# Optimization experiments

Measured on AMD Instinct MI355X. Metric: run time of the kernel, lower is better.

Reference implementation:

```python
import jax, jax.numpy as jnp
import numpy as np

COMMITMENT_COST = 0.25
DECAY = 0.99
EPSILON = 1e-05


def setup_inputs() -> dict:
    key = jax.random.key(0)
    k1, k2, k3 = jax.random.split(key, 3)
    B, C, H, W = 64, 64, 64, 64  # C == embedding_dim
    K, D = 1024, 64
    return {
        "inputs": jax.random.normal(k1, (B, C, H, W), dtype=jnp.float32),
        "weight": jax.random.normal(k2, (K, D), dtype=jnp.float32),
        "ema_cluster_size": jnp.ones((K,), dtype=jnp.float32),
        "ema_w": jax.random.normal(k3, (K, D), dtype=jnp.float32),
    }


def reference(inputs, weight, ema_cluster_size, ema_w):
    K, D = weight.shape
    # NCHW -> NHWC, flatten to [N, D]
    x = jnp.transpose(inputs, (0, 2, 3, 1))
    flat = x.reshape(-1, D)
    # squared L2 distances to all codebook entries: [N, K]
    distances = (
        jnp.sum(flat * flat, axis=1, keepdims=True)
        + jnp.sum(weight * weight, axis=1)
        - 2.0 * flat @ weight.T
    )
    idx = jnp.argmin(distances, axis=1)  # [N]
    # training-mode EMA update (replaces the one-hot scatter + matmuls with segment sums)
    counts = jax.ops.segment_sum(jnp.ones_like(idx, dtype=flat.dtype), idx, num_segments=K)
    dw = jax.ops.segment_sum(flat, idx, num_segments=K)  # encodings.T @ flat_input
    cs = ema_cluster_size * DECAY + (1.0 - DECAY) * counts
    n = jnp.sum(cs)
    cs = (cs + EPSILON) / (n + K * EPSILON) * n  # Laplace smoothing
    ew = ema_w * DECAY + (1.0 - DECAY) * dw
    new_weight = ew / cs[:, None]
    # quantize with the UPDATED codebook (matches in-place torch order)
    quantized = new_weight[idx].reshape(x.shape)
    e_latent_loss = jnp.mean(jnp.square(jax.lax.stop_gradient(quantized) - x))
    loss = COMMITMENT_COST * e_latent_loss
    quantized_st = x + jax.lax.stop_gradient(quantized - x)  # straight-through
    return loss, jnp.transpose(quantized_st, (0, 3, 1, 2)), idx[:, None]
```

## Files before the change

kernel.cpp:

```cpp
#include <hip/hip_runtime.h>

#define K_CODES 1024
#define D_DIM   64
#define N_ROWS  262144
#define HW      4096
#define CHW     262144
#define N_ELEM  16777216
#define DECAY   0.99f
#define OMD     0.01f
#define EPS_F   1e-05f
#define MARGIN_BF 0.008f
#define FLAG_CAP 32768
#define SEG_CAP  2048
#define NHB      64
#define BROWS    128

typedef __attribute__((ext_vector_type(8))) short bf16x8;
typedef __attribute__((ext_vector_type(4))) float f32x4;

constexpr size_t OFF_LOSS    = 0;
constexpr size_t OFF_FLAGCNT = 8;
constexpr size_t OFF_DONE    = 12;
constexpr size_t ZERO_BYTES  = 64;
constexpr size_t OFF_W2F     = 64;
constexpr size_t OFF_W2D     = 4160;
constexpr size_t OFF_CS     = 12352;
constexpr size_t OFF_GOFF    = 16448;
constexpr size_t OFF_DW      = 20608;
constexpr size_t OFF_NEWW    = 282752;
constexpr size_t OFF_IDX     = 544896;
constexpr size_t OFF_HISTB   = 1593472;
constexpr size_t OFF_SORT    = 1855616;
constexpr size_t OFF_FLAGS   = 1855616;
constexpr size_t OFF_WFRAG   = 1986688;

__device__ __forceinline__ short f2bf(float f) {
    unsigned u = __float_as_uint(f);
    u += 0x7fffu + ((u >> 16) & 1u);
    return (short)(u >> 16);
}
__device__ __forceinline__ float bf2f(short h) {
    return __uint_as_float(((unsigned)(unsigned short)h) << 16);
}

__device__ __forceinline__ void gload_lds16(const float4* g, void* l) {
    __builtin_amdgcn_global_load_lds(
        (const __attribute__((address_space(1))) void*)g,
        (__attribute__((address_space(3))) void*)l, 16, 0, 0);
}

__global__ __launch_bounds__(256) void prep_kernel(
    const float* __restrict__ w, short* __restrict__ wfrag,
    float* __restrict__ w2f, double* __restrict__ w2d) {
    int t = threadIdx.x;
    if (blockIdx.x < 32) {
        int gid = blockIdx.x * 256 + t;
        int j = gid >> 7, h = (gid >> 6) & 1, L = gid & 63;
        int code = j * 16 + (L & 15);
        int kb = h * 32 + ((L >> 4) << 3);
        const float* wp = w + code * D_DIM + kb;
        short hi[8], lo[8];
#pragma unroll
        for (int i = 0; i < 8; ++i) {
            float v = wp[i];
            short hb = f2bf(v);
            hi[i] = hb;
            lo[i] = f2bf(v - bf2f(hb));
        }
        short* dh = wfrag + (size_t)(((j * 2 + h) * 2 + 0) * 64 + L) * 8;
        short* dl = wfrag + (size_t)(((j * 2 + h) * 2 + 1) * 64 + L) * 8;
#pragma unroll
        for (int i = 0; i < 8; ++i) { dh[i] = hi[i]; dl[i] = lo[i]; }
    } else {
        int k = (blockIdx.x - 32) * 256 + t;
        const float* wk = w + k * D_DIM;
        float sf = 0.f; double sd = 0.0;
#pragma unroll
        for (int d = 0; d < D_DIM; ++d) {
            float wv = wk[d];
            sf = fmaf(wv, wv, sf);
            sd = fma((double)wv, (double)wv, sd);
        }
        w2f[k] = sf; w2d[k] = sd;
    }
}

__global__ __launch_bounds__(256) __attribute__((amdgpu_waves_per_eu(2, 4)))
void argmin_kernel(
    const float* __restrict__ inp, const short* __restrict__ wfrag,
    const float* __restrict__ w2f, int* __restrict__ idx_ws,
    float* __restrict__ out_idx_f, float* __restrict__ xt,
    int* __restrict__ flagcnt, int* __restrict__ flaglist) {
    __shared__ float w2s[K_CODES];
    __shared__ alignas(16) char smem_u[64 * 68 * 4];
    __shared__ alignas(16) short bufA[8192];
    float (*xs)[68] = (float (*)[68])smem_u;
    short* bufB = (short*)smem_u;

    int t = threadIdx.x;
    ((float4*)w2s)[t] = ((const float4*)w2f)[t];

    int rowbase = blockIdx.x * BROWS;
    int b = rowbase >> 12, hwb = rowbase & (HW - 1);
    const float* xp = inp + (size_t)b * CHW + hwb;
    int lane = t & 63, wave = t >> 6;
    int q = lane >> 4, col = lane & 15;

    bf16x8 aH[2][2], aL[2][2];

    for (int p = 0; p < 2; ++p) {
#pragma unroll
        for (int it = 0; it < 16; ++it) {
            int d = wave * 16 + it;
            xs[lane][d] = xp[(size_t)d * HW + p * 64 + lane];
        }
        __syncthreads();

        float4* xt4 = (float4*)(xt + (size_t)(rowbase + p * 64) * D_DIM);
#pragma unroll
        for (int i2 = 0; i2 < 4; ++i2) {
            int c2 = t + i2 * 256;
            xt4[c2] = ((const float4*)xs[c2 >> 4])[c2 & 15];
        }

        if ((wave >> 1) == p) {
#pragma unroll
            for (int s2 = 0; s2 < 2; ++s2) {
                int rl = (wave & 1) * 32 + s2 * 16 + col;
#pragma unroll
                for (int h = 0; h < 2; ++h) {
#pragma unroll
                    for (int i = 0; i < 8; ++i) {
                        float v = xs[rl][h * 32 + q * 8 + i];
                        short hb = f2bf(v);
                        aH[s2][h][i] = hb;
                        aL[s2][h][i] = f2bf(v - bf2f(hb));
                    }
                }
            }
        }
        __syncthreads();
    }

    float best[2][4], best2[2][4];
#pragma unroll
    for (int s2 = 0; s2 < 2; ++s2)
#pragma unroll
        for (int r = 0; r < 4; ++r) { best[s2][r] = 3.4e38f; best2[s2][r] = 3.4e38f; }
    const float4* wsrc = (const float4*)wfrag;

    {
        const float4* src = wsrc + t;
        char* nb = (char*)bufA + wave * 1024;
#pragma unroll
        for (int i2 = 0; i2 < 4; ++i2)
            gload_lds16(src + i2 * 256, nb + i2 * 4096);
    }

    for (int st = 0; st < 16; ++st) {
        asm volatile("s_waitcnt vmcnt(0)" ::: "memory");
        __syncthreads();
        if (st < 15) {
            const float4* src = wsrc + (size_t)(st + 1) * 1024 + t;
            char* nb = ((st & 1) ? (char*)bufA : (char*)bufB) + wave * 1024;
#pragma unroll
            for (int i2 = 0; i2 < 4; ++i2)
                gload_lds16(src + i2 * 256, nb + i2 * 4096);
        }
        const bf16x8* wt = (const bf16x8*)((st & 1) ? bufB : bufA);

#pragma unroll
        for (int jj = 0; jj < 4; ++jj) {
            int j = st * 4 + jj;
            bf16x8 bh0 = wt[(jj * 4 + 0) * 64 + lane];
            bf16x8 bl0 = wt[(jj * 4 + 1) * 64 + lane];
            bf16x8 bh1 = wt[(jj * 4 + 2) * 64 + lane];
            bf16x8 bl1 = wt[(jj * 4 + 3) * 64 + lane];
            f32x4 acc0 = {0.f, 0.f, 0.f, 0.f};
            f32x4 acc1 = {0.f, 0.f, 0.f, 0.f};
            acc0 = __builtin_amdgcn_mfma_f32_16x16x32_bf16(aL[0][0], bh0, acc0, 0, 0, 0);
            acc1 = __builtin_amdgcn_mfma_f32_16x16x32_bf16(aL[1][0], bh0, acc1, 0, 0, 0);
            acc0 = __builtin_amdgcn_mfma_f32_16x16x32_bf16(aL[0][1], bh1, acc0, 0, 0, 0);
            acc1 = __builtin_amdgcn_mfma_f32_16x16x32_bf16(aL[1][1], bh1, acc1, 0, 0, 0);
            acc0 = __builtin_amdgcn_mfma_f32_16x16x32_bf16(aH[0][0], bl0, acc0, 0, 0, 0);
            acc1 = __builtin_amdgcn_mfma_f32_16x16x32_bf16(aH[1][0], bl0, acc1, 0, 0, 0);
            acc0 = __builtin_amdgcn_mfma_f32_16x16x32_bf16(aH[0][1], bl1, acc0, 0, 0, 0);
            acc1 = __builtin_amdgcn_mfma_f32_16x16x32_bf16(aH[1][1], bl1, acc1, 0, 0, 0);
            acc0 = __builtin_amdgcn_mfma_f32_16x16x32_bf16(aH[0][0], bh0, acc0, 0, 0, 0);
            acc1 = __builtin_amdgcn_mfma_f32_16x16x32_bf16(aH[1][0], bh0, acc1, 0, 0, 0);
            acc0 = __builtin_amdgcn_mfma_f32_16x16x32_bf16(aH[0][1], bh1, acc0, 0, 0, 0);
            acc1 = __builtin_amdgcn_mfma_f32_16x16x32_bf16(aH[1][1], bh1, acc1, 0, 0, 0);
            float w2c = w2s[j * 16 + col];
#pragma unroll
            for (int s2 = 0; s2 < 2; ++s2) {
#pragma unroll
                for (int r = 0; r < 4; ++r) {
                    float s = fmaf(-2.f, (s2 ? acc1 : acc0)[r], w2c);
                    float key = __int_as_float(
                        (__float_as_int(s) & ~63) | j);
                    best2[s2][r] = fminf(best2[s2][r], fmaxf(key, best[s2][r]));
                    best[s2][r]  = fminf(best[s2][r], key);
                }
            }
        }
    }

    int bk[2][4];
#pragma unroll
    for (int s2 = 0; s2 < 2; ++s2)
#pragma unroll
        for (int r = 0; r < 4; ++r)
            bk[s2][r] = ((__float_as_int(best[s2][r]) & 63) << 4) | col;

#pragma unroll
    for (int m = 1; m < 16; m <<= 1) {
#pragma unroll
        for (int s2 = 0; s2 < 2; ++s2) {
#pragma unroll
            for (int r = 0; r < 4; ++r) {
                float ob  = __shfl_xor(best[s2][r], m, 64);
                float ob2 = __shfl_xor(best2[s2][r], m, 64);
                int   obk = __shfl_xor(bk[s2][r], m, 64);
                float nb2 = fminf(fminf(best2[s2][r], ob2),
                                  fmaxf(best[s2][r], ob));
                int   nbk = ob < best[s2][r] ? obk
                            : (best[s2][r] < ob ? bk[s2][r]
                                                : min(bk[s2][r], obk));
                best[s2][r]  = fminf(best[s2][r], ob);
                best2[s2][r] = nb2;
                bk[s2][r]    = nbk;
            }
        }
    }

    if (col == 0) {
#pragma unroll
        for (int s2 = 0; s2 < 2; ++s2) {
#pragma unroll
            for (int r = 0; r < 4; ++r) {
                int row = rowbase + wave * 32 + s2 * 16 + q * 4 + r;
                idx_ws[row]    = bk[s2][r];
                out_idx_f[row] = (float)bk[s2][r];
                if (best2[s2][r] - best[s2][r] < MARGIN_BF) {
                    int pos = atomicAdd(flagcnt, 1);
                    if (pos < FLAG_CAP) flaglist[pos] = row;
                }
            }
        }
    }
}

__global__ __launch_bounds__(256) void refine_kernel(
    const float* __restrict__ xt, const float* __restrict__ weight,
    const double* __restrict__ w2d, int* __restrict__ idx_ws,
    float* __restrict__ out_idx_f, const int* __restrict__ flagcnt,
    const int* __restrict__ flaglist) {
    __shared__ float sx[4][64];
    int cnt = *flagcnt;
    if (cnt > FLAG_CAP) cnt = FLAG_CAP;
    int t = threadIdx.x, lane = t & 63, wave = t >> 6;

    for (int r = blockIdx.x * 4 + wave; r < cnt; r += gridDim.x * 4) {
        int row = flaglist[r];
        sx[wave][lane] = xt[(size_t)row * D_DIM + lane];
        asm volatile("s_waitcnt lgkmcnt(0)" ::: "memory");

        double bd = 1.0e300; int bi = 0;
        int k0 = lane * 16;
#pragma unroll 4
        for (int c = 0; c < 16; ++c) {
            int k = k0 + c;
            const float4* wk4 = (const float4*)(weight + (size_t)k * D_DIM);
            double dot = 0.0;
#pragma unroll
            for (int d4 = 0; d4 < 16; ++d4) {
                float4 wv = wk4[d4];
                dot = fma((double)wv.x, (double)sx[wave][d4 * 4 + 0], dot);
                dot = fma((double)wv.y, (double)sx[wave][d4 * 4 + 1], dot);
                dot = fma((double)wv.z, (double)sx[wave][d4 * 4 + 2], dot);
                dot = fma((double)wv.w, (double)sx[wave][d4 * 4 + 3], dot);
            }
            double dist = w2d[k] - 2.0 * dot;
            if (dist < bd) { bd = dist; bi = k; }
        }
#pragma unroll
        for (int m = 1; m < 64; m <<= 1) {
            double od = __shfl_xor(bd, m, 64);
            int    oi = __shfl_xor(bi, m, 64);
            if (od < bd || (od == bd && oi < bi)) { bd = od; bi = oi; }
        }
        if (lane == 0 && bi != idx_ws[row]) {
            idx_ws[row]    = bi;
            out_idx_f[row] = (float)bi;
        }
    }
}

__global__ __launch_bounds__(256) void hist_kernel(
    const int* __restrict__ idx_ws, int* __restrict__ histb) {
    __shared__ int h[K_CODES];
    int t = threadIdx.x, b = blockIdx.x;
    for (int i = t; i < K_CODES; i += 256) h[i] = 0;
    __syncthreads();
    const int4* idx4 = (const int4*)idx_ws + b * 1024;
#pragma unroll
    for (int i = 0; i < 4; ++i) {
        int4 c = idx4[t + i * 256];
        atomicAdd(&h[c.x], 1); atomicAdd(&h[c.y], 1);
        atomicAdd(&h[c.z], 1); atomicAdd(&h[c.w], 1);
    }
    __syncthreads();
    for (int i = t; i < K_CODES; i += 256) histb[b * K_CODES + i] = h[i];
}

__global__ __launch_bounds__(1024) void scan_kernel(
    int* __restrict__ histb, int* __restrict__ goff,
    const float* __restrict__ ema_cs, float* __restrict__ csbuf) {
    __shared__ int pre[K_CODES];
    __shared__ float red[K_CODES];
    int k = threadIdx.x;

    int s = 0;
    for (int b = 0; b < NHB; ++b) {
        int v = histb[b * K_CODES + k];
        histb[b * K_CODES + k] = s;
        s += v;
    }
    int cnt = s;

    pre[k] = cnt;
    __syncthreads();
    for (int d = 1; d < K_CODES; d <<= 1) {
        int v = (k >= d) ? pre[k - d] : 0;
        __syncthreads();
        if (k >= d) pre[k] += v;
        __syncthreads();
    }
    int base = pre[k] - cnt;
    goff[k] = base;
    if (k == K_CODES - 1) goff[K_CODES] = pre[k];

    for (int b = 0; b < NHB; ++b) histb[b * K_CODES + k] += base;

    float cs = ema_cs[k] * DECAY + OMD * (float)cnt;
    red[k] = cs;
    __syncthreads();
    for (int s2 = 512; s2 > 0; s2 >>= 1) {
        if (k < s2) red[k] += red[k + s2];
        __syncthreads();
    }
    float n = red[0];
    csbuf[k] = (cs + EPS_F) / (n + (float)K_CODES * EPS_F) * n;
}

__global__ __launch_bounds__(256) void scatter_kernel(
    const int* __restrict__ idx_ws, const int* __restrict__ histb,
    int* __restrict__ sorted) {
    __shared__ int cur[K_CODES];
    int t = threadIdx.x, b = blockIdx.x;
    for (int i = t; i < K_CODES; i += 256) cur[i] = histb[b * K_CODES + i];
    __syncthreads();
    const int4* idx4 = (const int4*)idx_ws + b * 1024;
#pragma unroll
    for (int i = 0; i < 4; ++i) {
        int4 c = idx4[t + i * 256];
        int r0 = (b * 1024 + t + i * 256) * 4;
        sorted[atomicAdd(&cur[c.x], 1)] = r0 + 0;
        sorted[atomicAdd(&cur[c.y], 1)] = r0 + 1;
        sorted[atomicAdd(&cur[c.z], 1)] = r0 + 2;
        sorted[atomicAdd(&cur[c.w], 1)] = r0 + 3;
    }
}

__global__ __launch_bounds__(256) void dwred_kernel(
    const float* __restrict__ xt, const int* __restrict__ sorted,
    const int* __restrict__ goff, const float* __restrict__ ema_w,
    const float* __restrict__ csbuf, float* __restrict__ new_w) {
    __shared__ int   rows[SEG_CAP];
    __shared__ float red[256];
    int k = blockIdx.x, t = threadIdx.x;
    int base = goff[k];
    int cnt = goff[k + 1] - base;
    int cc = cnt > SEG_CAP ? SEG_CAP : cnt;

    for (int i = t; i < cc; i += 256) rows[i] = sorted[base + i];
    __syncthreads();

    int d = t & 63, sub = t >> 6;
    float a0 = 0.f, a1 = 0.f;
    int i = sub;
    for (; i + 4 < cc; i += 8) {
        a0 += xt[(size_t)rows[i] * D_DIM + d];
        a1 += xt[(size_t)rows[i + 4] * D_DIM + d];
    }
    for (; i < cc; i += 4) a0 += xt[(size_t)rows[i] * D_DIM + d];
    red[t] = a0 + a1;
    __syncthreads();
    if (t < 64) {
        float dwv = red[t] + red[t + 64] + red[t + 128] + red[t + 192];
        new_w[k * D_DIM + t] =
            (ema_w[k * D_DIM + t] * DECAY + OMD * dwv) / csbuf[k];
    }
}

__global__ __launch_bounds__(256) void out_kernel(
    const float* __restrict__ inp, const float* __restrict__ new_w,
    const int* __restrict__ idx_ws, float* __restrict__ out,
    double* __restrict__ loss_acc, int* __restrict__ done_cnt) {
    int row = blockIdx.x * 256 + threadIdx.x;
    int b  = row >> 12;
    int hw = row & (HW - 1);
    const float* xp = inp + (size_t)b * CHW + hw;
    float* op = out + 1 + (size_t)b * CHW + hw;

    int k = idx_ws[row];
    const float* q = new_w + k * D_DIM;

    float lsum = 0.f;
#pragma unroll
    for (int d = 0; d < D_DIM; ++d) {
        float xv = xp[(size_t)d * HW];
        float qv = q[d];
        float diff = qv - xv;
        lsum = fmaf(diff, diff, lsum);
        op[(size_t)d * HW] = xv + diff;
    }

    __shared__ double lred[256];
    lred[threadIdx.x] = (double)lsum;
    __syncthreads();
    for (int s = 128; s > 0; s >>= 1) {
        if (threadIdx.x < s) lred[threadIdx.x] += lred[threadIdx.x + s];
        __syncthreads();
    }
    if (threadIdx.x == 0) {
        atomicAdd(loss_acc, lred[0]);
        __threadfence();
        int old = atomicAdd(done_cnt, 1);
        if (old == (int)gridDim.x - 1) {
            double v = atomicAdd(loss_acc, 0.0);
            out[0] = (float)(0.25 * (v / (double)N_ELEM));
        }
    }
}

extern "C" void kernel_launch(void* const* d_in, const int* in_sizes, int n_in,
                              void* d_out, int out_size, void* d_ws, size_t ws_size,
                              hipStream_t stream) {
    const float* inp    = (const float*)d_in[0];
    const float* weight = (const float*)d_in[1];
    const float* ema_cs = (const float*)d_in[2];
    const float* ema_w  = (const float*)d_in[3];
    float* out = (float*)d_out;

    char* ws = (char*)d_ws;
    double* loss_acc = (double*)(ws + OFF_LOSS);
    int*    flagcnt  = (int*)(ws + OFF_FLAGCNT);
    int*    done_cnt = (int*)(ws + OFF_DONE);
    float*  w2f      = (float*)(ws + OFF_W2F);
    double* w2d      = (double*)(ws + OFF_W2D);
    float*  csbuf    = (float*)(ws + OFF_CS);
    int*    goff     = (int*)(ws + OFF_GOFF);
    float*  new_w    = (float*)(ws + OFF_NEWW);
    int*    idx_ws   = (int*)(ws + OFF_IDX);
    int*    histb    = (int*)(ws + OFF_HISTB);
    int*    sorted   = (int*)(ws + OFF_SORT);
    int*    flaglist = (int*)(ws + OFF_FLAGS);
    short*  wfrag    = (short*)(ws + OFF_WFRAG);

    float* xt        = out + 1;
    float* out_idx_f = out + 1 + (size_t)N_ELEM;

    hipMemsetAsync(ws, 0, ZERO_BYTES, stream);

    prep_kernel<<<36, 256, 0, stream>>>(weight, wfrag, w2f, w2d);

    argmin_kernel<<<N_ROWS / BROWS, 256, 0, stream>>>(
        inp, wfrag, w2f, idx_ws, out_idx_f, xt, flagcnt, flaglist);

    refine_kernel<<<256, 256, 0, stream>>>(
        xt, weight, w2d, idx_ws, out_idx_f, flagcnt, flaglist);

    hist_kernel<<<NHB, 256, 0, stream>>>(idx_ws, histb);

    scan_kernel<<<1, 1024, 0, stream>>>(histb, goff, ema_cs, csbuf);

    scatter_kernel<<<NHB, 256, 0, stream>>>(idx_ws, histb, sorted);

    dwred_kernel<<<K_CODES, 256, 0, stream>>>(xt, sorted, goff, ema_w, csbuf, new_w);

    out_kernel<<<N_ROWS / 256, 256, 0, stream>>>(inp, new_w, idx_ws, out,
                                                 loss_acc, done_cnt);
}
```

Measured before the change: 436.1 us.

## Enlarge argmin row tile, fold norm into MFMA init, fuse scan into hist

The argmin kernel now handles 256 rows per block, so each wave keeps 64 rows (4 A-fragment sets) and every codebook fragment loaded from LDS is reused across more rows. The accumulator starts at -0.5*||w||^2, so the argmin becomes a max of x·w - 0.5||w||^2 and the per-element fma disappears, and the ambiguity margin is halved to match the halved scale. The scan kernel is merged into the last-finishing hist block through an atomic done counter. The memset is replaced by zeroing inside prep_kernel, and refine gets twice as many blocks. The cost is higher register pressure and fewer argmin blocks, plus a serial tail in the last hist block.

```diff
diff --git a/kernel.cpp b/kernel.cpp
--- a/kernel.cpp
+++ b/kernel.cpp
@@ -9,11 +9,11 @@
 #define DECAY   0.99f
 #define OMD     0.01f
 #define EPS_F   1e-05f
-#define MARGIN_BF 0.008f
+#define MARGIN_ACC 0.004f
 #define FLAG_CAP 32768
 #define SEG_CAP  2048
 #define NHB      64
-#define BROWS    128
+#define BROWS    256
 
 typedef __attribute__((ext_vector_type(8))) short bf16x8;
 typedef __attribute__((ext_vector_type(4))) float f32x4;
@@ -21,12 +21,11 @@
 constexpr size_t OFF_LOSS    = 0;
 constexpr size_t OFF_FLAGCNT = 8;
 constexpr size_t OFF_DONE    = 12;
-constexpr size_t ZERO_BYTES  = 64;
+constexpr size_t OFF_HDONE   = 16;
 constexpr size_t OFF_W2F     = 64;
 constexpr size_t OFF_W2D     = 4160;
 constexpr size_t OFF_CS     = 12352;
 constexpr size_t OFF_GOFF    = 16448;
-constexpr size_t OFF_DW      = 20608;
 constexpr size_t OFF_NEWW    = 282752;
 constexpr size_t OFF_IDX     = 544896;
 constexpr size_t OFF_HISTB   = 1593472;
@@ -51,8 +50,10 @@
 
 __global__ __launch_bounds__(256) void prep_kernel(
     const float* __restrict__ w, short* __restrict__ wfrag,
-    float* __restrict__ w2f, double* __restrict__ w2d) {
+    float* __restrict__ w2f, double* __restrict__ w2d,
+    int* __restrict__ zero16) {
     int t = threadIdx.x;
+    if (blockIdx.x == 35 && t < 8) zero16[t] = 0;
     if (blockIdx.x < 32) {
         int gid = blockIdx.x * 256 + t;
         int j = gid >> 7, h = (gid >> 6) & 1, L = gid & 63;
@@ -85,7 +86,7 @@
     }
 }
 
-__global__ __launch_bounds__(256) __attribute__((amdgpu_waves_per_eu(2, 4)))
+__global__ __launch_bounds__(256) __attribute__((amdgpu_waves_per_eu(3, 4)))
 void argmin_kernel(
     const float* __restrict__ inp, const short* __restrict__ wfrag,
     const float* __restrict__ w2f, int* __restrict__ idx_ws,
@@ -106,9 +107,10 @@
     int lane = t & 63, wave = t >> 6;
     int q = lane >> 4, col = lane & 15;
 
-    bf16x8 aH[2][2], aL[2][2];
-
-    for (int p = 0; p < 2; ++p) {
+    bf16x8 aH[4][2], aL[4][2];
+
+#pragma unroll
+    for (int p = 0; p < 4; ++p) {
 #pragma unroll
         for (int it = 0; it < 16; ++it) {
             int d = wave * 16 + it;
@@ -123,10 +125,10 @@
             xt4[c2] = ((const float4*)xs[c2 >> 4])[c2 & 15];
         }
 
-        if ((wave >> 1) == p) {
-#pragma unroll
-            for (int s2 = 0; s2 < 2; ++s2) {
-                int rl = (wave & 1) * 32 + s2 * 16 + col;
+        if (wave == p) {
+#pragma unroll
+            for (int s2 = 0; s2 < 4; ++s2) {
+                int rl = s2 * 16 + col;
 #pragma unroll
                 for (int h = 0; h < 2; ++h) {
 #pragma unroll
@@ -142,11 +144,11 @@
         __syncthreads();
     }
 
-    float best[2][4], best2[2][4];
-#pragma unroll
-    for (int s2 = 0; s2 < 2; ++s2)
-#pragma unroll
-        for (int r = 0; r < 4; ++r) { best[s2][r] = 3.4e38f; best2[s2][r] = 3.4e38f; }
+    float best[4][4], best2[4][4];
+#pragma unroll
+    for (int s2 = 0; s2 < 4; ++s2)
+#pragma unroll
+        for (int r = 0; r < 4; ++r) { best[s2][r] = -3.4e38f; best2[s2][r] = -3.4e38f; }
     const float4* wsrc = (const float4*)wfrag;
 
     {
@@ -156,6 +158,8 @@
         for (int i2 = 0; i2 < 4; ++i2)
             gload_lds16(src + i2 * 256, nb + i2 * 4096);
     }
+
+#define MFMA16(A, B, C) __builtin_amdgcn_mfma_f32_16x16x32_bf16(A, B, C, 0, 0, 0)
 
     for (int st = 0; st < 16; ++st) {
         asm volatile("s_waitcnt vmcnt(0)" ::: "memory");
@@ -176,38 +180,38 @@
             bf16x8 bl0 = wt[(jj * 4 + 1) * 64 + lane];
             bf16x8 bh1 = wt[(jj * 4 + 2) * 64 + lane];
             bf16x8 bl1 = wt[(jj * 4 + 3) * 64 + lane];
-            f32x4 acc0 = {0.f, 0.f, 0.f, 0.f};
-            f32x4 acc1 = {0.f, 0.f, 0.f, 0.f};
-            acc0 = __builtin_amdgcn_mfma_f32_16x16x32_bf16(aL[0][0], bh0, acc0, 0, 0, 0);
-            acc1 = __builtin_amdgcn_mfma_f32_16x16x32_bf16(aL[1][0], bh0, acc1, 0, 0, 0);
-            acc0 = __builtin_amdgcn_mfma_f32_16x16x32_bf16(aL[0][1], bh1, acc0, 0, 0, 0);
-            acc1 = __builtin_amdgcn_mfma_f32_16x16x32_bf16(aL[1][1], bh1, acc1, 0, 0, 0);
-            acc0 = __builtin_amdgcn_mfma_f32_16x16x32_bf16(aH[0][0], bl0, acc0, 0, 0, 0);
-            acc1 = __builtin_amdgcn_mfma_f32_16x16x32_bf16(aH[1][0], bl0, acc1, 0, 0, 0);
-            acc0 = __builtin_amdgcn_mfma_f32_16x16x32_bf16(aH[0][1], bl1, acc0, 0, 0, 0);
-            acc1 = __builtin_amdgcn_mfma_f32_16x16x32_bf16(aH[1][1], bl1, acc1, 0, 0, 0);
-            acc0 = __builtin_amdgcn_mfma_f32_16x16x32_bf16(aH[0][0], bh0, acc0, 0, 0, 0);
-            acc1 = __builtin_amdgcn_mfma_f32_16x16x32_bf16(aH[1][0], bh0, acc1, 0, 0, 0);
-            acc0 = __builtin_amdgcn_mfma_f32_16x16x32_bf16(aH[0][1], bh1, acc0, 0, 0, 0);
-            acc1 = __builtin_amdgcn_mfma_f32_16x16x32_bf16(aH[1][1], bh1, acc1, 0, 0, 0);
-            float w2c = w2s[j * 16 + col];
-#pragma unroll
-            for (int s2 = 0; s2 < 2; ++s2) {
+            float cj = -0.5f * w2s[j * 16 + col];
+            f32x4 ac0 = {cj, cj, cj, cj}, ac1 = {cj, cj, cj, cj};
+            f32x4 ac2 = {cj, cj, cj, cj}, ac3 = {cj, cj, cj, cj};
+            ac0 = MFMA16(aL[0][0], bh0, ac0); ac1 = MFMA16(aL[1][0], bh0, ac1);
+            ac2 = MFMA16(aL[2][0], bh0, ac2); ac3 = MFMA16(aL[3][0], bh0, ac3);
+            ac0 = MFMA16(aL[0][1], bh1, ac0); ac1 = MFMA16(aL[1][1], bh1, ac1);
+            ac2 = MFMA16(aL[2][1], bh1, ac2); ac3 = MFMA16(aL[3][1], bh1, ac3);
+            ac0 = MFMA16(aH[0][0], bl0, ac0); ac1 = MFMA16(aH[1][0], bl0, ac1);
+            ac2 = MFMA16(aH[2][0], bl0, ac2); ac3 = MFMA16(aH[3][0], bl0, ac3);
+            ac0 = MFMA16(aH[0][1], bl1, ac0); ac1 = MFMA16(aH[1][1], bl1, ac1);
+            ac2 = MFMA16(aH[2][1], bl1, ac2); ac3 = MFMA16(aH[3][1], bl1, ac3);
+            ac0 = MFMA16(aH[0][0], bh0, ac0); ac1 = MFMA16(aH[1][0], bh0, ac1);
+            ac2 = MFMA16(aH[2][0], bh0, ac2); ac3 = MFMA16(aH[3][0], bh0, ac3);
+            ac0 = MFMA16(aH[0][1], bh1, ac0); ac1 = MFMA16(aH[1][1], bh1, ac1);
+            ac2 = MFMA16(aH[2][1], bh1, ac2); ac3 = MFMA16(aH[3][1], bh1, ac3);
+#pragma unroll
+            for (int s2 = 0; s2 < 4; ++s2) {
+                f32x4 av = (s2 == 0) ? ac0 : (s2 == 1) ? ac1 : (s2 == 2) ? ac2 : ac3;
 #pragma unroll
                 for (int r = 0; r < 4; ++r) {
-                    float s = fmaf(-2.f, (s2 ? acc1 : acc0)[r], w2c);
-                    float key = __int_as_float(
-                        (__float_as_int(s) & ~63) | j);
-                    best2[s2][r] = fminf(best2[s2][r], fmaxf(key, best[s2][r]));
-                    best[s2][r]  = fminf(best[s2][r], key);
+                    float key = __int_as_float((__float_as_int(av[r]) & ~63) | j);
+                    best2[s2][r] = fmaxf(best2[s2][r], fminf(best[s2][r], key));
+                    best[s2][r]  = fmaxf(best[s2][r], key);
                 }
             }
         }
     }
-
-    int bk[2][4];
-#pragma unroll
-    for (int s2 = 0; s2 < 2; ++s2)
+#undef MFMA16
+
+    int bk[4][4];
+#pragma unroll
+    for (int s2 = 0; s2 < 4; ++s2)
 #pragma unroll
         for (int r = 0; r < 4; ++r)
             bk[s2][r] = ((__float_as_int(best[s2][r]) & 63) << 4) | col;
@@ -215,18 +219,18 @@
 #pragma unroll
     for (int m = 1; m < 16; m <<= 1) {
 #pragma unroll
-        for (int s2 = 0; s2 < 2; ++s2) {
+        for (int s2 = 0; s2 < 4; ++s2) {
 #pragma unroll
             for (int r = 0; r < 4; ++r) {
                 float ob  = __shfl_xor(best[s2][r], m, 64);
                 float ob2 = __shfl_xor(best2[s2][r], m, 64);
                 int   obk = __shfl_xor(bk[s2][r], m, 64);
-                float nb2 = fminf(fminf(best2[s2][r], ob2),
-                                  fmaxf(best[s2][r], ob));
-                int   nbk = ob < best[s2][r] ? obk
-                            : (best[s2][r] < ob ? bk[s2][r]
+                float nb2 = fmaxf(fmaxf(best2[s2][r], ob2),
+                                  fminf(best[s2][r], ob));
+                int   nbk = ob > best[s2][r] ? obk
+                            : (best[s2][r] > ob ? bk[s2][r]
                                                 : min(bk[s2][r], obk));
-                best[s2][r]  = fminf(best[s2][r], ob);
+                best[s2][r]  = fmaxf(best[s2][r], ob);
                 best2[s2][r] = nb2;
                 bk[s2][r]    = nbk;
             }
@@ -235,13 +239,13 @@
 
     if (col == 0) {
 #pragma unroll
-        for (int s2 = 0; s2 < 2; ++s2) {
+        for (int s2 = 0; s2 < 4; ++s2) {
 #pragma unroll
             for (int r = 0; r < 4; ++r) {
-                int row = rowbase + wave * 32 + s2 * 16 + q * 4 + r;
+                int row = rowbase + wave * 64 + s2 * 16 + q * 4 + r;
                 idx_ws[row]    = bk[s2][r];
                 out_idx_f[row] = (float)bk[s2][r];
-                if (best2[s2][r] - best[s2][r] < MARGIN_BF) {
+                if (best[s2][r] - best2[s2][r] < MARGIN_ACC) {
                     int pos = atomicAdd(flagcnt, 1);
                     if (pos < FLAG_CAP) flaglist[pos] = row;
                 }
@@ -297,7 +301,9 @@
 }
 
 __global__ __launch_bounds__(256) void hist_kernel(
-    const int* __restrict__ idx_ws, int* __restrict__ histb) {
+    const int* __restrict__ idx_ws, int* __restrict__ histb,
+    int* __restrict__ hist_done, const float* __restrict__ ema_cs,
+    float* __restrict__ csbuf, int* __restrict__ goff) {
     __shared__ int h[K_CODES];
     int t = threadIdx.x, b = blockIdx.x;
     for (int i = t; i < K_CODES; i += 256) h[i] = 0;
@@ -311,46 +317,61 @@
     }
     __syncthreads();
     for (int i = t; i < K_CODES; i += 256) histb[b * K_CODES + i] = h[i];
-}
-
-__global__ __launch_bounds__(1024) void scan_kernel(
-    int* __restrict__ histb, int* __restrict__ goff,
-    const float* __restrict__ ema_cs, float* __restrict__ csbuf) {
-    __shared__ int pre[K_CODES];
-    __shared__ float red[K_CODES];
-    int k = threadIdx.x;
-
-    int s = 0;
-    for (int b = 0; b < NHB; ++b) {
-        int v = histb[b * K_CODES + k];
-        histb[b * K_CODES + k] = s;
-        s += v;
-    }
-    int cnt = s;
-
-    pre[k] = cnt;
-    __syncthreads();
-    for (int d = 1; d < K_CODES; d <<= 1) {
-        int v = (k >= d) ? pre[k - d] : 0;
-        __syncthreads();
-        if (k >= d) pre[k] += v;
-        __syncthreads();
-    }
-    int base = pre[k] - cnt;
-    goff[k] = base;
-    if (k == K_CODES - 1) goff[K_CODES] = pre[k];
-
-    for (int b = 0; b < NHB; ++b) histb[b * K_CODES + k] += base;
-
-    float cs = ema_cs[k] * DECAY + OMD * (float)cnt;
-    red[k] = cs;
-    __syncthreads();
-    for (int s2 = 512; s2 > 0; s2 >>= 1) {
-        if (k < s2) red[k] += red[k + s2];
-        __syncthreads();
-    }
-    float n = red[0];
-    csbuf[k] = (cs + EPS_F) / (n + (float)K_CODES * EPS_F) * n;
+
+    __shared__ int amLast;
+    if (t == 0) {
+        __threadfence();
+        amLast = (atomicAdd(hist_done, 1) == NHB - 1);
+    }
+    __syncthreads();
+    if (!amLast) return;
+
+    __shared__ int   pre[256];
+    __shared__ float redf[256];
+    int cnt4[4]; int mysum = 0;
+#pragma unroll
+    for (int c = 0; c < 4; ++c) {
+        int k = t * 4 + c;
+        int s = 0;
+        for (int b2 = 0; b2 < NHB; ++b2) {
+            int v = histb[b2 * K_CODES + k];
+            histb[b2 * K_CODES + k] = s;
+            s += v;
+        }
+        cnt4[c] = s; mysum += s;
+    }
+    pre[t] = mysum;
+    __syncthreads();
+    for (int d = 1; d < 256; d <<= 1) {
+        int v = (t >= d) ? pre[t - d] : 0;
+        __syncthreads();
+        if (t >= d) pre[t] += v;
+        __syncthreads();
+    }
+    int kb = pre[t] - mysum;
+    float css[4]; float mycs = 0.f;
+#pragma unroll
+    for (int c = 0; c < 4; ++c) {
+        int k = t * 4 + c;
+        goff[k] = kb;
+        for (int b2 = 0; b2 < NHB; ++b2) histb[b2 * K_CODES + k] += kb;
+        kb += cnt4[c];
+        css[c] = ema_cs[k] * DECAY + OMD * (float)cnt4[c];
+        mycs += css[c];
+    }
+    if (t == 255) goff[K_CODES] = kb;
+    redf[t] = mycs;
+    __syncthreads();
+    for (int s2 = 128; s2 > 0; s2 >>= 1) {
+        if (t < s2) redf[t] += redf[t + s2];
+        __syncthreads();
+    }
+    float n = redf[0];
+#pragma unroll
+    for (int c = 0; c < 4; ++c) {
+        int k = t * 4 + c;
+        csbuf[k] = (css[c] + EPS_F) / (n + (float)K_CODES * EPS_F) * n;
+    }
 }
 
 __global__ __launch_bounds__(256) void scatter_kernel(
@@ -457,6 +478,7 @@
     double* loss_acc = (double*)(ws + OFF_LOSS);
     int*    flagcnt  = (int*)(ws + OFF_FLAGCNT);
     int*    done_cnt = (int*)(ws + OFF_DONE);
+    int*    hdone    = (int*)(ws + OFF_HDONE);
     float*  w2f      = (float*)(ws + OFF_W2F);
     double* w2d      = (double*)(ws + OFF_W2D);
     float*  csbuf    = (float*)(ws + OFF_CS);
@@ -471,19 +493,16 @@
     float* xt        = out + 1;
     float* out_idx_f = out + 1 + (size_t)N_ELEM;
 
-    hipMemsetAsync(ws, 0, ZERO_BYTES, stream);
-
-    prep_kernel<<<36, 256, 0, stream>>>(weight, wfrag, w2f, w2d);
+    prep_kernel<<<36, 256, 0, stream>>>(weight, wfrag, w2f, w2d, (int*)ws);
 
     argmin_kernel<<<N_ROWS / BROWS, 256, 0, stream>>>(
         inp, wfrag, w2f, idx_ws, out_idx_f, xt, flagcnt, flaglist);
 
-    refine_kernel<<<256, 256, 0, stream>>>(
+    refine_kernel<<<512, 256, 0, stream>>>(
         xt, weight, w2d, idx_ws, out_idx_f, flagcnt, flaglist);
 
-    hist_kernel<<<NHB, 256, 0, stream>>>(idx_ws, histb);
-
-    scan_kernel<<<1, 1024, 0, stream>>>(histb, goff, ema_cs, csbuf);
+    hist_kernel<<<NHB, 256, 0, stream>>>(idx_ws, histb, hdone,
+                                         ema_cs, csbuf, goff);
 
     scatter_kernel<<<NHB, 256, 0, stream>>>(idx_ws, histb, sorted);
 
```

Result: slower. 468.4 us (+7.4%).
